# Optimization experiments

Hardware: AMD Instinct MI355X
Metric: run time of the kernel (lower is better)

## Reference

```python
import jax, jax.numpy as jnp
import numpy as np

B, N, K, A = 2, 4096, 20, 12
DIMS = [32, 64, 128, 256, 512]
POOL_RATE, POOL_K = 4, 4


def knn_index(v, k):
    # v: (b, n, 3) -> (b, n, k) nearest neighbors, self excluded
    d2 = jnp.sum(v * v, axis=-1)
    dist = d2[:, :, None] + d2[:, None, :] - 2.0 * jnp.einsum('bnd,bmd->bnm', v, v)
    _, idx = jax.lax.top_k(-dist, k + 1)
    return idx[:, :, 1:]


def gather_pos(v, idx):
    return jax.vmap(lambda vv, ii: vv[ii])(v, idx)  # (b, n, k, 3)


def gather_fea(fm, idx):
    return jax.vmap(lambda f, ii: f[:, ii, :])(fm, idx)  # (b, c, n, k, a)


def nbr_dirs(v, idx):
    d = gather_pos(v, idx) - v[:, :, None, :]
    return d / (jnp.linalg.norm(d, axis=-1, keepdims=True) + 1e-8)


def conv_surface(idx, v, K0):
    # K0: (C0, A, 3) learned direction kernels; output (b, C0, n, A)
    d = nbr_dirs(v, idx)  # (b,n,k,3)
    theta = jax.nn.relu(jnp.einsum('bnkd,cad->bnkca', d, K0))
    return jnp.transpose(jnp.max(theta, axis=2), (0, 2, 1, 3))


def equi_conv(idx, v, fm, dirs, Wc, bc, Ws):
    # fm: (b, cin, n, a) -> (b, cout, n, a)
    d = nbr_dirs(v, idx)
    theta = jax.nn.relu(jnp.einsum('bnkd,ad->bnka', d, dirs))  # (b,n,k,a)
    fn = gather_fea(fm, idx)  # (b,cin,n,k,a)
    fs = jnp.einsum('bcnka,co->bonka', fn, Ws) * theta[:, None]
    fs = jnp.max(fs, axis=3)  # max over neighbors -> (b,cout,n,a)
    fc = jnp.einsum('bcna,co->bona', fm, Wc) + bc[None, :, None, None]
    return fc + fs


def batchnorm(x, g, b):
    m = jnp.mean(x, axis=(0, 2, 3), keepdims=True)
    var = jnp.var(x, axis=(0, 2, 3), keepdims=True)
    return (x - m) * jax.lax.rsqrt(var + 1e-5) * g[None, :, None, None] + b[None, :, None, None]


def pool(v, fm):
    idx = knn_index(v, POOL_K)
    fn = jnp.max(gather_fea(fm, idx), axis=3)
    fm_p = jnp.maximum(fm, fn)
    sel = jnp.arange(0, v.shape[1], POOL_RATE)  # strided subsample
    return v[:, sel], fm_p[:, :, sel]


def fea_of(fm):
    return jnp.transpose(jnp.max(fm, axis=-1), (0, 2, 1))  # (b,n,c)


def setup_inputs() -> dict:
    key = jax.random.key(0)
    ks = iter(jax.random.split(key, 32))
    p = {'vertices': jax.random.normal(next(ks), (B, N, 3), jnp.float32)}
    p['K0'] = jax.random.normal(next(ks), (DIMS[0], A, 3), jnp.float32) * 0.1
    for i, (ci, co) in enumerate(zip(DIMS[:4], DIMS[1:]), start=1):
        s = 1.0 / np.sqrt(ci).astype(np.float32)
        p[f'dirs{i}'] = jax.random.normal(next(ks), (A, 3), jnp.float32) * 0.1
        p[f'Wc{i}'] = jax.random.normal(next(ks), (ci, co), jnp.float32) * s
        p[f'bc{i}'] = jnp.zeros((co,), jnp.float32)
        p[f'Ws{i}'] = jax.random.normal(next(ks), (ci, co), jnp.float32) * s
    for i, c in enumerate([DIMS[1], DIMS[2], DIMS[3]], start=1):
        p[f'g{i}'] = jnp.ones((c,), jnp.float32)
        p[f'b{i}'] = jnp.zeros((c,), jnp.float32)
    return p


def reference(vertices, K0, dirs1, Wc1, bc1, Ws1, dirs2, Wc2, bc2, Ws2,
              dirs3, Wc3, bc3, Ws3, dirs4, Wc4, bc4, Ws4,
              g1, b1, g2, b2, g3, b3):
    idx = knn_index(vertices, K)
    fm0 = jax.nn.relu(conv_surface(idx, vertices, K0))
    fm1 = jax.nn.relu(batchnorm(equi_conv(idx, vertices, fm0, dirs1, Wc1, bc1, Ws1), g1, b1))
    v1, fmp1 = pool(vertices, fm1)
    idx1 = knn_index(v1, min(K, v1.shape[1] // 8))
    fm2 = jax.nn.relu(batchnorm(equi_conv(idx1, v1, fmp1, dirs2, Wc2, bc2, Ws2), g2, b2))
    fm3 = jax.nn.relu(batchnorm(equi_conv(idx1, v1, fm2, dirs3, Wc3, bc3, Ws3), g3, b3))
    v2, fmp2 = pool(v1, fm3)
    idx2 = knn_index(v2, min(K, v2.shape[1] // 8))
    fm4 = equi_conv(idx2, v2, fmp2, dirs4, Wc4, bc4, Ws4)
    return fea_of(fm0), fea_of(fm1), fea_of(fm2), fea_of(fm3), fea_of(fm4)
```

## Files before the change

### kernel.cpp

```cpp
#include <hip/hip_runtime.h>
#include <hip/hip_bf16.h>
#include <math.h>

typedef unsigned short u16;
typedef unsigned long long u64;
#define DEV static __device__ __forceinline__

constexpr int Bz = 2, N0 = 4096, N1 = 1024, N2 = 256, KNN = 20, NA = 12;
constexpr int C0 = 32, C1 = 64, C2 = 128, C3 = 256, C4 = 512;
constexpr int BNG = 32;

constexpr size_t OFF_V0F   = 0;
constexpr size_t OFF_V1F   = 32768;
constexpr size_t OFF_V2F   = 40960;
constexpr size_t OFF_K0F   = 43008;
constexpr size_t OFF_DIRS  = 44160;
constexpr size_t OFF_WC    = 44304;
constexpr size_t OFF_WS    = 218384;
constexpr size_t OFF_BC    = 392464;
constexpr size_t OFF_BN    = 393424;
constexpr size_t OFF_FLAG  = 394832;
constexpr size_t OFF_IDX0  = 394848;
constexpr size_t OFF_IDX1  = 558688;
constexpr size_t OFF_IDX2  = 599648;
constexpr size_t OFF_PART  = 609888;
constexpr size_t PART_SZ   = 28672;
constexpr size_t OFF_HALF  = OFF_PART + PART_SZ;

constexpr size_t HA = 0;
constexpr size_t HB = 3145728;
constexpr size_t HG = 9437184;
constexpr size_t HP = HG + 3145728;

constexpr size_t OUT0 = 0;
constexpr size_t OUT1 = OUT0 + (size_t)Bz*N0*C0;
constexpr size_t OUT2 = OUT1 + (size_t)Bz*N0*C1;
constexpr size_t OUT3 = OUT2 + (size_t)Bz*N1*C2;
constexpr size_t OUT4 = OUT3 + (size_t)Bz*N1*C3;

DEV float b2f(u16 v) { return __uint_as_float(((unsigned int)v) << 16); }
DEV u16 f2b(float f) {
  unsigned int u = __float_as_uint(f);
  unsigned int lsb = (u >> 16) & 1u;
  return (u16)((u + 0x7fffu + lsb) >> 16);
}
DEV unsigned packb(float a, float b) {
  return (unsigned)f2b(a) | ((unsigned)f2b(b) << 16);
}

DEV u64 shflx64(u64 v, int m) {
  int lo = __shfl_xor((int)(unsigned)v, m, 64);
  int hi = __shfl_xor((int)(unsigned)(v >> 32), m, 64);
  return ((u64)(unsigned)hi << 32) | (unsigned)lo;
}
DEV int mbcnt64(u64 m) {
  return __builtin_amdgcn_mbcnt_hi((unsigned)(m >> 32),
         __builtin_amdgcn_mbcnt_lo((unsigned)m, 0));
}

DEV void st12(float* dst, const float* v) {
  float4 a{v[0],v[1],v[2],v[3]}, b{v[4],v[5],v[6],v[7]}, c{v[8],v[9],v[10],v[11]};
  ((float4*)dst)[0] = a; ((float4*)dst)[1] = b; ((float4*)dst)[2] = c;
}
DEV void st12(u16* dst, const float* v) {
  uint2 a{packb(v[0],v[1]), packb(v[2],v[3])};
  uint2 b{packb(v[4],v[5]), packb(v[6],v[7])};
  uint2 c{packb(v[8],v[9]), packb(v[10],v[11])};
  ((uint2*)dst)[0] = a; ((uint2*)dst)[1] = b; ((uint2*)dst)[2] = c;
}

struct InPtrs { const void* p[24]; };

__global__ void eq_convert_all(InPtrs in, float* ws) {
  __shared__ int sflag;
  {
    const u16* v = (const u16*)in.p[0];
    if (threadIdx.x < 64) {
      int bad = 0;
      #pragma unroll
      for (int j = 0; j < 4; ++j) {
        unsigned u = v[threadIdx.x*4 + j];
        int ex = (u >> 7) & 0xFF;
        bad += (((u & 0x7FFFu) != 0u) && (ex < 64 || ex > 191)) ? 1 : 0;
      }
      int tot = bad;
      #pragma unroll
      for (int s = 32; s > 0; s >>= 1) tot += __shfl_xor(tot, s, 64);
      if (threadIdx.x == 0) sflag = (tot >= 8) ? 1 : 0;
    }
    __syncthreads();
  }
  int f32mode = sflag;
  int t = blockIdx.x * blockDim.x + threadIdx.x;
  if (t < Bz*N0) {
    float x, y, z;
    if (f32mode) { const float* v = (const float*)in.p[0]; x=v[t*3]; y=v[t*3+1]; z=v[t*3+2]; }
    else { const u16* v = (const u16*)in.p[0]; x=b2f(v[t*3]); y=b2f(v[t*3+1]); z=b2f(v[t*3+2]); }
    float4 o; o.x=x; o.y=y; o.z=z; o.w=(x*x + y*y) + z*z;
    ((float4*)(ws + OFF_V0F))[t] = o;
    int b = t / N0, i = t % N0;
    if ((i & 3) == 0)  ((float4*)(ws + OFF_V1F))[b*N1 + (i >> 2)] = o;
    if ((i & 15) == 0) ((float4*)(ws + OFF_V2F))[b*N2 + (i >> 4)] = o;
    return;
  }
  int r = t - Bz*N0;
  if (r >= 351312) {
    int z = r - 351312;
    if (z < (int)PART_SZ) ws[OFF_PART + z] = 0.f;
    return;
  }
  const int cnt[23] = {1152, 36,2048,64,2048, 36,8192,128,8192,
                       36,32768,256,32768, 36,131072,512,131072,
                       64,64,128,128,256,256};
  const size_t off[23] = {OFF_K0F,
    OFF_DIRS+0,   OFF_WC+0,     OFF_BC+0,   OFF_WS+0,
    OFF_DIRS+36,  OFF_WC+2048,  OFF_BC+64,  OFF_WS+2048,
    OFF_DIRS+72,  OFF_WC+10240, OFF_BC+192, OFF_WS+10240,
    OFF_DIRS+108, OFF_WC+43008, OFF_BC+448, OFF_WS+43008,
    OFF_BN+0, OFF_BN+64, OFF_BN+128, OFF_BN+256, OFF_BN+384, OFF_BN+640};
  for (int i = 0; i < 23; ++i) {
    if (r < cnt[i]) {
      float val = f32mode ? ((const float*)in.p[i+1])[r] : b2f(((const u16*)in.p[i+1])[r]);
      ws[off[i] + r] = val;
      return;
    }
    r -= cnt[i];
  }
}

DEV unsigned cand_ud(const float4 vq, const float4 vc) {
  float dt = fmaf(vq.x, vc.x, fmaf(vq.y, vc.y, vq.z*vc.z));
  float d  = fmaf(-2.0f, dt, vq.w + vc.w);
  unsigned u = __float_as_uint(d);
  return u ^ ((unsigned)(((int)u) >> 31) | 0x80000000u);
}

#define INSA(u,c) do { bool lt1=(u)<dA1, lt2=(u)<dA2, lt3=(u)<dA3, lt4=(u)<dA4; \
  dA4=lt3?dA3:(lt4?(u):dA4); iA4=lt3?iA3:(lt4?(c):iA4); \
  dA3=lt2?dA2:(lt3?(u):dA3); iA3=lt2?iA2:(lt3?(c):iA3); \
  dA2=lt1?dA1:(lt2?(u):dA2); iA2=lt1?iA1:(lt2?(c):iA2); \
  dA1=lt1?(u):dA1;           iA1=lt1?(c):iA1; } while(0)
#define INSB(u,c) do { bool lt1=(u)<dB1, lt2=(u)<dB2, lt3=(u)<dB3, lt4=(u)<dB4; \
  dB4=lt3?dB3:(lt4?(u):dB4); iB4=lt3?iB3:(lt4?(c):iB4); \
  dB3=lt2?dB2:(lt3?(u):dB3); iB3=lt2?iB2:(lt3?(c):iB3); \
  dB2=lt1?dB1:(lt2?(u):dB2); iB2=lt1?iB1:(lt2?(c):iB2); \
  dB1=lt1?(u):dB1;           iB1=lt1?(c):iB1; } while(0)

#define CMP1(uu,cc) do { bool sel=(uu)<=p; u64 m=__ballot(sel); \
  int pos = base2 + mbcnt64(m); \
  if (sel && pos < 128) selw[pos] = ((u64)(uu) << 32) | (unsigned)(cc); \
  base2 += __popcll(m); } while(0)

template<int NPTS>
DEV void knn_body(int blk, const float4* __restrict__ vf, int* __restrict__ idx_out,
                  char* smem) {
  constexpr int CPL = NPTS/64;
  constexpr int HC  = CPL/2;
  int wave = threadIdx.x >> 6, lane = threadIdx.x & 63;
  u64* selw = (u64*)smem + wave*128;
  int* extrw = (int*)(smem + 4*128*8) + wave*24;
  int qid = blk*4 + wave;
  int b = qid / NPTS, q = qid % NPTS;
  const float4* vb = vf + (size_t)b*NPTS;
  float4 vq = vb[q];

  unsigned dA1=~0u,dA2=~0u,dA3=~0u,dA4=~0u; int iA1=0,iA2=0,iA3=0,iA4=0;
  unsigned dB1=~0u,dB2=~0u,dB3=~0u,dB4=~0u; int iB1=0,iB2=0,iB3=0,iB4=0;

  if (CPL >= 8) {
    for (int jb = 0; jb < CPL; jb += 8) {
      int base = jb*64 + lane;
      float4 c0 = vb[base];
      float4 c1 = vb[base + 64];
      float4 c2 = vb[base + 128];
      float4 c3 = vb[base + 192];
      float4 c4 = vb[base + 256];
      float4 c5 = vb[base + 320];
      float4 c6 = vb[base + 384];
      float4 c7 = vb[base + 448];
      unsigned u0 = cand_ud(vq, c0);
      unsigned u1 = cand_ud(vq, c1);
      unsigned u2 = cand_ud(vq, c2);
      unsigned u3 = cand_ud(vq, c3);
      unsigned u4 = cand_ud(vq, c4);
      unsigned u5 = cand_ud(vq, c5);
      unsigned u6 = cand_ud(vq, c6);
      unsigned u7 = cand_ud(vq, c7);
      INSA(u0, base);       INSB(u1, base + 64);
      INSA(u2, base + 128); INSB(u3, base + 192);
      INSA(u4, base + 256); INSB(u5, base + 320);
      INSA(u6, base + 384); INSB(u7, base + 448);
    }
  } else {
    int base = lane;
    float4 c0 = vb[base];
    float4 c1 = vb[base + 64];
    float4 c2 = vb[base + 128];
    float4 c3 = vb[base + 192];
    unsigned u0 = cand_ud(vq, c0);
    unsigned u1 = cand_ud(vq, c1);
    unsigned u2 = cand_ud(vq, c2);
    unsigned u3 = cand_ud(vq, c3);
    INSA(u0, base);       INSB(u1, base + 64);
    INSA(u2, base + 128); INSB(u3, base + 192);
  }

  unsigned p = 0;
  for (int bit = 31; bit >= 0; --bit) {
    unsigned T = p | (1u << bit);
    int cnt = __popcll(__ballot(dA1 < T)) + __popcll(__ballot(dA2 < T))
            + __popcll(__ballot(dA3 < T)) + __popcll(__ballot(dA4 < T))
            + __popcll(__ballot(dB1 < T)) + __popcll(__ballot(dB2 < T))
            + __popcll(__ballot(dB3 < T)) + __popcll(__ballot(dB4 < T));
    if (cnt < KNN+1) p = T;
  }
  size_t obase = (size_t)qid*KNN;
  bool need_fb = (HC > 4) &&
                 ((__ballot(dA4 <= p) | __ballot(dB4 <= p)) != 0ULL);

  if (!need_fb) {
    bool pA1=dA1<=p, pA2=dA2<=p, pA3=dA3<=p, pA4=dA4<=p;
    bool pB1=dB1<=p, pB2=dB2<=p, pB3=dB3<=p, pB4=dB4<=p;
    u64 m1=__ballot(pA1), m2=__ballot(pA2), m3=__ballot(pA3), m4=__ballot(pA4);
    u64 m5=__ballot(pB1), m6=__ballot(pB2), m7=__ballot(pB3), m8=__ballot(pB4);
    int c1=__popcll(m1), c2=__popcll(m2), c3=__popcll(m3), c4=__popcll(m4);
    int c5=__popcll(m5), c6=__popcll(m6), c7=__popcll(m7), c8=__popcll(m8);
    int S = ((c1+c2)+(c3+c4)) + ((c5+c6)+(c7+c8));
    if (S > 127) need_fb = true;
    else {
      int o1=c1, o2=o1+c2, o3=o2+c3, o4=o3+c4, o5=o4+c5, o6=o5+c6, o7=o6+c7;
      if (pA1) selw[mbcnt64(m1)]      = ((u64)dA1 << 32) | (unsigned)iA1;
      if (pA2) selw[o1 + mbcnt64(m2)] = ((u64)dA2 << 32) | (unsigned)iA2;
      if (pA3) selw[o2 + mbcnt64(m3)] = ((u64)dA3 << 32) | (unsigned)iA3;
      if (pA4) selw[o3 + mbcnt64(m4)] = ((u64)dA4 << 32) | (unsigned)iA4;
      if (pB1) selw[o4 + mbcnt64(m5)] = ((u64)dB1 << 32) | (unsigned)iB1;
      if (pB2) selw[o5 + mbcnt64(m6)] = ((u64)dB2 << 32) | (unsigned)iB2;
      if (pB3) selw[o6 + mbcnt64(m7)] = ((u64)dB3 << 32) | (unsigned)iB3;
      if (pB4) selw[o7 + mbcnt64(m8)] = ((u64)dB4 << 32) | (unsigned)iB4;
      for (int sl = lane; sl < S; sl += 64) {
        u64 mykey = selw[sl];
        int rank = 0;
        for (int j2 = 0; j2 < S; ++j2) rank += (selw[j2] < mykey) ? 1 : 0;
        if (rank >= 1 && rank <= KNN)
          idx_out[obase + rank - 1] = (int)(unsigned)(mykey & 0xFFFFFFFFu);
      }
    }
  }
  if (need_fb && CPL >= 8) {
    int base2 = 0;
    for (int jb = 0; jb < CPL; jb += 8) {
      int bidx = jb*64 + lane;
      float4 c0 = vb[bidx];
      float4 c1 = vb[bidx + 64];
      float4 c2 = vb[bidx + 128];
      float4 c3 = vb[bidx + 192];
      float4 c4 = vb[bidx + 256];
      float4 c5 = vb[bidx + 320];
      float4 c6 = vb[bidx + 384];
      float4 c7 = vb[bidx + 448];
      unsigned u0 = cand_ud(vq, c0);
      unsigned u1 = cand_ud(vq, c1);
      unsigned u2 = cand_ud(vq, c2);
      unsigned u3 = cand_ud(vq, c3);
      unsigned u4 = cand_ud(vq, c4);
      unsigned u5 = cand_ud(vq, c5);
      unsigned u6 = cand_ud(vq, c6);
      unsigned u7 = cand_ud(vq, c7);
      CMP1(u0, bidx);       CMP1(u1, bidx + 64);
      CMP1(u2, bidx + 128); CMP1(u3, bidx + 192);
      CMP1(u4, bidx + 256); CMP1(u5, bidx + 320);
      CMP1(u6, bidx + 384); CMP1(u7, bidx + 448);
    }
    if (base2 <= 127) {
      int S = base2;
      for (int sl = lane; sl < S; sl += 64) {
        u64 mykey = selw[sl];
        int rank = 0;
        for (int j2 = 0; j2 < S; ++j2) rank += (selw[j2] < mykey) ? 1 : 0;
        if (rank >= 1 && rank <= KNN)
          idx_out[obase + rank - 1] = (int)(unsigned)(mykey & 0xFFFFFFFFu);
      }
    } else {
      const u64 KINF = ~0ULL;
      u64 K1=KINF, K2=KINF, K3=KINF, K4=KINF;
      for (int j = 0; j < CPL; ++j) {
        int c = j*64 + lane;
        u64 k = ((u64)cand_ud(vq, vb[c]) << 32) | (unsigned)c;
        bool lt1 = k < K1, lt2 = k < K2, lt3 = k < K3, lt4 = k < K4;
        K4 = lt3 ? K3 : (lt4 ? k : K4);
        K3 = lt2 ? K2 : (lt3 ? k : K3);
        K2 = lt1 ? K1 : (lt2 ? k : K2);
        K1 = lt1 ? k  : K1;
      }
      for (int r = 0; r < KNN+1; ++r) {
        u64 g = K1;
        #pragma unroll
        for (int s = 32; s; s >>= 1) { u64 o = shflx64(g, s); g = (o < g) ? o : g; }
        int gidx = (int)(unsigned)(g & 0xFFFFFFFFu);
        if (lane == 0) {
          extrw[r] = gidx;
          if (r > 0) idx_out[obase + r - 1] = gidx;
        }
        if (r < KNN && lane == (gidx & 63)) {
          K1 = K2; K2 = K3; K3 = K4; K4 = KINF;
          if (K1 == KINF) {
            for (int j = 0; j < CPL; ++j) {
              int c = j*64 + lane;
              u64 k = ((u64)cand_ud(vq, vb[c]) << 32) | (unsigned)c;
              bool ex = false;
              for (int e = 0; e <= r; ++e) ex |= (extrw[e] == c);
              if (!ex) {
                bool lt1 = k < K1, lt2 = k < K2, lt3 = k < K3, lt4 = k < K4;
                K4 = lt3 ? K3 : (lt4 ? k : K4);
                K3 = lt2 ? K2 : (lt3 ? k : K3);
                K2 = lt1 ? K1 : (lt2 ? k : K2);
                K1 = lt1 ? k  : K1;
              }
            }
          }
        }
      }
    }
  }
}

__global__ __launch_bounds__(256) void eq_knn_all(
    const float4* __restrict__ v0, int* __restrict__ i0,
    const float4* __restrict__ v1, int* __restrict__ i1,
    const float4* __restrict__ v2, int* __restrict__ i2) {
  __shared__ __align__(16) char smem[4*128*8 + 4*24*4];
  int blk = blockIdx.x;
  constexpr int NB0 = Bz*N0/4, NB1 = Bz*N1/4;
  if (blk < NB0)            knn_body<N0>(blk, v0, i0, smem);
  else if (blk < NB0+NB1)   knn_body<N1>(blk - NB0, v1, i1, smem);
  else                      knn_body<N2>(blk - NB0 - NB1, v2, i2, smem);
}

__global__ __launch_bounds__(128) void eq_conv_surface(
    const float4* __restrict__ v0f, const int* __restrict__ idx0,
    const float* __restrict__ K0f, u16* __restrict__ fm0, float* __restrict__ out0) {
  int bq = blockIdx.x;
  int b = bq >> 12;
  __shared__ float dk[KNN][3];
  __shared__ float row[C0*NA];
  int tid = threadIdx.x;
  if (tid < KNN) {
    int m = idx0[(size_t)bq*KNN + tid];
    float4 vq = v0f[bq];
    float4 vm = v0f[(size_t)b*N0 + m];
    float dx = vm.x - vq.x, dy = vm.y - vq.y, dz = vm.z - vq.z;
    float nrm = sqrtf((dx*dx + dy*dy) + dz*dz) + 1e-8f;
    dk[tid][0] = dx/nrm; dk[tid][1] = dy/nrm; dk[tid][2] = dz/nrm;
  }
  __syncthreads();
  for (int t4 = tid; t4 < C0*NA/4; t4 += 128) {
    const float* kd = K0f + (size_t)t4*12;
    float4 k0 = *(const float4*)(kd);
    float4 k1 = *(const float4*)(kd + 4);
    float4 k2 = *(const float4*)(kd + 8);
    float m0=0.f, m1=0.f, m2=0.f, m3=0.f;
    #pragma unroll
    for (int k = 0; k < KNN; ++k) {
      float dx = dk[k][0], dy = dk[k][1], dz = dk[k][2];
      m0 = fmaxf(m0, (dx*k0.x + dy*k0.y) + dz*k0.z);
      m1 = fmaxf(m1, (dx*k0.w + dy*k1.x) + dz*k1.y);
      m2 = fmaxf(m2, (dx*k1.z + dy*k1.w) + dz*k2.x);
      m3 = fmaxf(m3, (dx*k2.y + dy*k2.z) + dz*k2.w);
    }
    uint2 r; r.x = packb(m0, m1); r.y = packb(m2, m3);
    ((uint2*)fm0)[(size_t)bq*(C0*NA/4) + t4] = r;
    row[4*t4+0] = m0; row[4*t4+1] = m1; row[4*t4+2] = m2; row[4*t4+3] = m3;
  }
  __syncthreads();
  if (tid < C0) {
    float m = row[tid*NA];
    #pragma unroll
    for (int a = 1; a < NA; ++a) m = fmaxf(m, row[tid*NA + a]);
    out0[(size_t)bq*C0 + tid] = m;
  }
}

template<int CI, int CO, typename TO>
__global__ __launch_bounds__(256) void eq_linear4(
    const u16* __restrict__ in, const float* __restrict__ Wc,
    const float* __restrict__ Ws, const float* __restrict__ bias,
    TO* __restrict__ fc, u16* __restrict__ g) {
  constexpr int PPB = 512 / CO;
  constexpr int RS = CI*NA + 4;
  __shared__ float lds[PPB*RS];
  int tid = threadIdx.x;
  int mat = blockIdx.x & 1;
  int pt0 = (blockIdx.x >> 1) * PPB;
  constexpr int E = PPB*CI*NA;
  for (int t = tid; t < E; t += 256) {
    int pt = t / (CI*NA), r = t % (CI*NA);
    lds[pt*RS + r] = b2f(in[((size_t)(pt0+pt))*CI*NA + r]);
  }
  __syncthreads();
  constexpr int TPP = CO/2;
  int opair = tid % TPP, pt = tid / TPP;
  int o0 = opair*2;
  const float* W = mat ? Ws : Wc;
  const float* row = lds + pt*RS;
  float a0[NA], a1[NA];
  #pragma unroll
  for (int a = 0; a < NA; ++a) { a0[a]=0.f; a1[a]=0.f; }
  #pragma unroll 4
  for (int c = 0; c < CI; ++c) {
    float2 w2 = *(const float2*)(W + (size_t)c*CO + o0);
    float4 i0 = *(const float4*)(row + c*NA);
    float4 i1 = *(const float4*)(row + c*NA + 4);
    float4 i2 = *(const float4*)(row + c*NA + 8);
    float iv[NA] = {i0.x,i0.y,i0.z,i0.w, i1.x,i1.y,i1.z,i1.w, i2.x,i2.y,i2.z,i2.w};
    #pragma unroll
    for (int a = 0; a < NA; ++a) {
      a0[a] += iv[a]*w2.x; a1[a] += iv[a]*w2.y;
    }
  }
  size_t ptg = pt0 + pt;
  if (mat == 0) {
    float b0 = bias[o0], b1 = bias[o0+1];
    #pragma unroll
    for (int a = 0; a < NA; ++a) { a0[a] += b0; a1[a] += b1; }
    st12(fc + ((size_t)ptg*CO + o0)*NA, a0);
    st12(fc + ((size_t)ptg*CO + o0 + 1)*NA, a1);
  } else {
    st12(g + ((size_t)ptg*CO + o0)*NA, a0);
    st12(g + ((size_t)ptg*CO + o0 + 1)*NA, a1);
  }
}

__global__ __launch_bounds__(256) void eq_fsmax(
    const u16* __restrict__ g, const float4* __restrict__ vf,
    const float* __restrict__ dirs, const int* __restrict__ idx,
    u16* __restrict__ out, float* __restrict__ part, int npts, int co) {
  int bq = blockIdx.x;
  int b = bq / npts;
  __shared__ float th[KNN*NA];
  __shared__ float dk[KNN][3];
  __shared__ int nb[KNN];
  __shared__ float sstat[2][C3];
  int tid = threadIdx.x;
  if (tid < KNN) {
    int m = idx[(size_t)bq*KNN + tid];
    nb[tid] = m;
    float4 vq = vf[bq];
    float4 vm = vf[(size_t)b*npts + m];
    float dx = vm.x - vq.x, dy = vm.y - vq.y, dz = vm.z - vq.z;
    float nrm = sqrtf((dx*dx + dy*dy) + dz*dz) + 1e-8f;
    dk[tid][0] = dx/nrm; dk[tid][1] = dy/nrm; dk[tid][2] = dz/nrm;
  }
  sstat[0][tid] = 0.f; sstat[1][tid] = 0.f;
  __syncthreads();
  if (tid < KNN*NA) {
    int k = tid / NA, a = tid % NA;
    float s = (dk[k][0]*dirs[a*3] + dk[k][1]*dirs[a*3+1]) + dk[k][2]*dirs[a*3+2];
    th[tid] = fmaxf(s, 0.f);
  }
  __syncthreads();
  int quarter = co*NA/4;
  uint2* dst = (uint2*)(out + (size_t)bq*co*NA);
  const uint2* gb = (const uint2*)(g + (size_t)b*npts*co*NA);
  for (int t4 = tid; t4 < quarter; t4 += 256) {
    int a = (4*t4) % NA;
    const float* tha = th + a;
    float m0=-3.0e38f, m1=-3.0e38f, m2=-3.0e38f, m3=-3.0e38f;
    #pragma unroll 5
    for (int k = 0; k < KNN; ++k) {
      uint2 pv = gb[(size_t)nb[k]*quarter + t4];
      float4 tv = *(const float4*)(tha + k*NA);
      m0 = fmaxf(m0, tv.x*b2f((u16)(pv.x)));
      m1 = fmaxf(m1, tv.y*b2f((u16)(pv.x >> 16)));
      m2 = fmaxf(m2, tv.z*b2f((u16)(pv.y)));
      m3 = fmaxf(m3, tv.w*b2f((u16)(pv.y >> 16)));
    }
    uint2 d = dst[t4];
    float v0 = b2f((u16)d.x) + m0;
    float v1 = b2f((u16)(d.x >> 16)) + m1;
    float v2 = b2f((u16)d.y) + m2;
    float v3 = b2f((u16)(d.y >> 16)) + m3;
    uint2 r; r.x = packb(v0, v1); r.y = packb(v2, v3);
    dst[t4] = r;
    int ch = t4 / 3;
    atomicAdd(&sstat[0][ch], (v0 + v1) + (v2 + v3));
    atomicAdd(&sstat[1][ch], (v0*v0 + v1*v1) + (v2*v2 + v3*v3));
  }
  __syncthreads();
  if (tid < co) {
    float* pg = part + (size_t)(bq & (BNG-1))*2*co;
    atomicAdd(&pg[tid], sstat[0][tid]);
    atomicAdd(&pg[co + tid], sstat[1][tid]);
  }
}

template<int SPL>
__global__ __launch_bounds__(256) void eq_fsmax_fea(
    const u16* __restrict__ g, const float* __restrict__ fcin,
    const float4* __restrict__ vf, const float* __restrict__ dirs,
    const int* __restrict__ idx, float* __restrict__ outfea,
    int npts, int co) {
  constexpr int CHUNK = C4 / SPL;
  int part = blockIdx.x % SPL;
  int bq = blockIdx.x / SPL;
  int b = bq / npts;
  __shared__ float th[KNN*NA];
  __shared__ float dk[KNN][3];
  __shared__ int nb[KNN];
  __shared__ float row[CHUNK*NA];
  int tid = threadIdx.x;
  if (tid < KNN) {
    int m = idx[(size_t)bq*KNN + tid];
    nb[tid] = m;
    float4 vq = vf[bq];
    float4 vm = vf[(size_t)b*npts + m];
    float dx = vm.x - vq.x, dy = vm.y - vq.y, dz = vm.z - vq.z;
    float nrm = sqrtf((dx*dx + dy*dy) + dz*dz) + 1e-8f;
    dk[tid][0] = dx/nrm; dk[tid][1] = dy/nrm; dk[tid][2] = dz/nrm;
  }
  __syncthreads();
  if (tid < KNN*NA) {
    int k = tid / NA, a = tid % NA;
    float s = (dk[k][0]*dirs[a*3] + dk[k][1]*dirs[a*3+1]) + dk[k][2]*dirs[a*3+2];
    th[tid] = fmaxf(s, 0.f);
  }
  __syncthreads();
  int o0 = part * CHUNK;
  const float4* fcr = (const float4*)(fcin + ((size_t)bq*co + o0)*NA);
  const uint2* gb = (const uint2*)(g + (size_t)b*npts*co*NA + (size_t)o0*NA);
  int gquarter = co*NA/4;
  for (int t4 = tid; t4 < CHUNK*NA/4; t4 += 256) {
    int a = (4*t4) % NA;
    const float* tha = th + a;
    float m0=-3.0e38f, m1=-3.0e38f, m2=-3.0e38f, m3=-3.0e38f;
    #pragma unroll 5
    for (int k = 0; k < KNN; ++k) {
      uint2 pv = gb[(size_t)nb[k]*gquarter + t4];
      float4 tv = *(const float4*)(tha + k*NA);
      m0 = fmaxf(m0, tv.x*b2f((u16)(pv.x)));
      m1 = fmaxf(m1, tv.y*b2f((u16)(pv.x >> 16)));
      m2 = fmaxf(m2, tv.z*b2f((u16)(pv.y)));
      m3 = fmaxf(m3, tv.w*b2f((u16)(pv.y >> 16)));
    }
    float4 fc4 = fcr[t4];
    row[4*t4+0] = fc4.x + m0;
    row[4*t4+1] = fc4.y + m1;
    row[4*t4+2] = fc4.z + m2;
    row[4*t4+3] = fc4.w + m3;
  }
  __syncthreads();
  for (int o = tid; o < CHUNK; o += 256) {
    float m = row[o*NA];
    #pragma unroll
    for (int a = 1; a < NA; ++a) m = fmaxf(m, row[o*NA + a]);
    outfea[(size_t)bq*co + o0 + o] = m;
  }
}

__global__ __launch_bounds__(256) void eq_bnrelu_fea(
    u16* __restrict__ fm, const float* __restrict__ part,
    const float* __restrict__ gamma, const float* __restrict__ beta,
    float* __restrict__ outfea, int npts, int co) {
  int bq = blockIdx.x;
  int tid = threadIdx.x;
  __shared__ float sc[C3], sh[C3];
  __shared__ float row[C3*NA];
  for (int o = tid; o < co; o += 256) {
    float s = 0.f, s2 = 0.f;
    for (int g = 0; g < BNG; ++g) {
      s  += part[(size_t)g*2*co + o];
      s2 += part[(size_t)g*2*co + co + o];
    }
    float cnt = (float)(Bz*npts*NA);
    float mean = s / cnt;
    float var = fmaxf(s2 / cnt - mean*mean, 0.f);
    float inv = 1.0f / sqrtf(var + 1e-5f);
    sc[o] = gamma[o] * inv;
    sh[o] = beta[o] - mean * gamma[o] * inv;
  }
  __syncthreads();
  uint2* p = (uint2*)(fm + (size_t)bq*co*NA);
  int quarter = co*NA/4;
  for (int t4 = tid; t4 < quarter; t4 += 256) {
    int o = (4*t4) / NA;
    float s = sc[o], h = sh[o];
    uint2 pv = p[t4];
    float v0 = fmaxf(b2f((u16)pv.x)*s + h, 0.f);
    float v1 = fmaxf(b2f((u16)(pv.x >> 16))*s + h, 0.f);
    float v2 = fmaxf(b2f((u16)pv.y)*s + h, 0.f);
    float v3 = fmaxf(b2f((u16)(pv.y >> 16))*s + h, 0.f);
    uint2 r; r.x = packb(v0, v1); r.y = packb(v2, v3);
    p[t4] = r;
    row[4*t4+0] = v0; row[4*t4+1] = v1; row[4*t4+2] = v2; row[4*t4+3] = v3;
  }
  __syncthreads();
  for (int o = tid; o < co; o += 256) {
    float m = row[o*NA];
    #pragma unroll
    for (int a = 1; a < NA; ++a) m = fmaxf(m, row[o*NA + a]);
    outfea[(size_t)bq*co + o] = m;
  }
}

__global__ __launch_bounds__(256) void eq_bnfea_pool(
    const u16* __restrict__ fm, const float* __restrict__ part,
    const float* __restrict__ gamma, const float* __restrict__ beta,
    const int* __restrict__ idx, float* __restrict__ outfea,
    u16* __restrict__ fmp, int npts, int co) {
  int bq = blockIdx.x;
  int b = bq / npts, q = bq % npts;
  int tid = threadIdx.x;
  __shared__ float sc[C3], sh[C3];
  __shared__ float row[C3*NA];
  __shared__ int nb[4];
  for (int o = tid; o < co; o += 256) {
    float s = 0.f, s2 = 0.f;
    for (int g = 0; g < BNG; ++g) {
      s  += part[(size_t)g*2*co + o];
      s2 += part[(size_t)g*2*co + co + o];
    }
    float cnt = (float)(Bz*npts*NA);
    float mean = s / cnt;
    float var = fmaxf(s2 / cnt - mean*mean, 0.f);
    float inv = 1.0f / sqrtf(var + 1e-5f);
    sc[o] = gamma[o] * inv;
    sh[o] = beta[o] - mean * gamma[o] * inv;
  }
  bool do_pool = ((q & 3) == 0);
  if (do_pool && tid < 4) nb[tid] = idx[(size_t)bq*KNN + tid];
  __syncthreads();
  int quarter = co*NA/4;
  const uint2* own = (const uint2*)(fm + (size_t)bq*co*NA);
  const uint2* base = (const uint2*)(fm + (size_t)b*npts*co*NA);
  uint2* dst = (uint2*)(fmp + ((size_t)b*(npts/4) + (q >> 2))*co*NA);
  for (int t4 = tid; t4 < quarter; t4 += 256) {
    int o = (4*t4) / NA;
    float s = sc[o], h = sh[o];
    uint2 pv = own[t4];
    float v0 = fmaxf(b2f((u16)pv.x)*s + h, 0.f);
    float v1 = fmaxf(b2f((u16)(pv.x >> 16))*s + h, 0.f);
    float v2 = fmaxf(b2f((u16)pv.y)*s + h, 0.f);
    float v3 = fmaxf(b2f((u16)(pv.y >> 16))*s + h, 0.f);
    row[4*t4+0] = v0; row[4*t4+1] = v1; row[4*t4+2] = v2; row[4*t4+3] = v3;
    if (do_pool) {
      float m0=v0, m1=v1, m2=v2, m3=v3;
      #pragma unroll
      for (int kk = 0; kk < 4; ++kk) {
        uint2 w = base[(size_t)nb[kk]*quarter + t4];
        m0 = fmaxf(m0, fmaxf(b2f((u16)w.x)*s + h, 0.f));
        m1 = fmaxf(m1, fmaxf(b2f((u16)(w.x >> 16))*s + h, 0.f));
        m2 = fmaxf(m2, fmaxf(b2f((u16)w.y)*s + h, 0.f));
        m3 = fmaxf(m3, fmaxf(b2f((u16)(w.y >> 16))*s + h, 0.f));
      }
      uint2 r; r.x = packb(m0, m1); r.y = packb(m2, m3);
      dst[t4] = r;
    }
  }
  __syncthreads();
  for (int o = tid; o < co; o += 256) {
    float m = row[o*NA];
    #pragma unroll
    for (int a = 1; a < NA; ++a) m = fmaxf(m, row[o*NA + a]);
    outfea[(size_t)bq*co + o] = m;
  }
}

extern "C" void kernel_launch(void* const* d_in, const int* in_sizes, int n_in,
                              void* d_out, int out_size, void* d_ws, size_t ws_size,
                              hipStream_t stream) {
  float* ws = (float*)d_ws;
  float* out = (float*)d_out;
  u16* arena = (u16*)(ws + OFF_HALF);

  InPtrs ip;
  for (int i = 0; i < 24; ++i) ip.p[i] = d_in[i];

  float4* v0f = (float4*)(ws + OFF_V0F);
  float4* v1f = (float4*)(ws + OFF_V1F);
  float4* v2f = (float4*)(ws + OFF_V2F);
  int* idx0 = (int*)(ws + OFF_IDX0);
  int* idx1 = (int*)(ws + OFF_IDX1);
  int* idx2 = (int*)(ws + OFF_IDX2);
  u16* bufA = arena + HA;
  u16* bufB = arena + HB;
  float* fc4f = (float*)(arena + HB);
  u16* bufG = arena + HG;
  u16* bufP = arena + HP;
  float* partA = ws + OFF_PART;
  float* partB = ws + OFF_PART + 4096;
  float* partC = ws + OFF_PART + 12288;
  const float* DIRS = ws + OFF_DIRS;

  {
    int total = Bz*N0 + 351312 + (int)PART_SZ;
    eq_convert_all<<<(total + 255)/256, 256, 0, stream>>>(ip, ws);
  }

  eq_knn_all<<<Bz*N0/4 + Bz*N1/4 + Bz*N2/4, 256, 0, stream>>>(v0f, idx0, v1f, idx1, v2f, idx2);
  eq_conv_surface<<<Bz*N0, 128, 0, stream>>>(v0f, idx0, ws + OFF_K0F, bufA, out + OUT0);

  eq_linear4<C0, C1, u16><<<(Bz*N0/8)*2, 256, 0, stream>>>(bufA, ws + OFF_WC + 0, ws + OFF_WS + 0,
                                                           ws + OFF_BC + 0, bufB, bufG);
  eq_fsmax<<<Bz*N0, 256, 0, stream>>>(bufG, v0f, DIRS + 0, idx0, bufB, partA, N0, C1);
  eq_bnfea_pool<<<Bz*N0, 256, 0, stream>>>(bufB, partA, ws + OFF_BN + 0, ws + OFF_BN + 64,
                                           idx0, out + OUT1, bufP, N0, C1);

  eq_linear4<C1, C2, u16><<<(Bz*N1/4)*2, 256, 0, stream>>>(bufP, ws + OFF_WC + 2048, ws + OFF_WS + 2048,
                                                           ws + OFF_BC + 64, bufA, bufG);
  eq_fsmax<<<Bz*N1, 256, 0, stream>>>(bufG, v1f, DIRS + 36, idx1, bufA, partB, N1, C2);
  eq_bnrelu_fea<<<Bz*N1, 256, 0, stream>>>(bufA, partB, ws + OFF_BN + 128, ws + OFF_BN + 256,
                                           out + OUT2, N1, C2);

  eq_linear4<C2, C3, u16><<<(Bz*N1/2)*2, 256, 0, stream>>>(bufA, ws + OFF_WC + 10240, ws + OFF_WS + 10240,
                                                           ws + OFF_BC + 192, bufB, bufG);
  eq_fsmax<<<Bz*N1, 256, 0, stream>>>(bufG, v1f, DIRS + 72, idx1, bufB, partC, N1, C3);
  eq_bnfea_pool<<<Bz*N1, 256, 0, stream>>>(bufB, partC, ws + OFF_BN + 384, ws + OFF_BN + 640,
                                           idx1, out + OUT3, bufP, N1, C3);

  eq_linear4<C3, C4, float><<<(Bz*N2)*2, 256, 0, stream>>>(bufP, ws + OFF_WC + 43008, ws + OFF_WS + 43008,
                                                           ws + OFF_BC + 448, fc4f, bufG);
  eq_fsmax_fea<4><<<Bz*N2*4, 256, 0, stream>>>(bufG, fc4f, v2f, DIRS + 108, idx2, out + OUT4, N2, C4);
}
```

Before: 442.9 us.

## Use bf16 MFMA with hi/lo weight split for equivariant linear layers

Replaces the scalar FP32 per-point linear kernels with MFMA 16x16x32 bf16 matrix-core kernels. A new prep kernel transposes each weight matrix and splits it into bf16 high and low parts, so two MFMAs per k-step keep near-fp32 accuracy on the weight side. Input tiles are staged in LDS, transposed to an (angle, point) by channel layout. Points per block change for most layers, and the extra weight-prep launch plus the scattered scalar output stores add cost.

```diff
diff --git a/kernel.cpp b/kernel.cpp
--- a/kernel.cpp
+++ b/kernel.cpp
@@ -31,6 +31,7 @@
 constexpr size_t HB = 3145728;
 constexpr size_t HG = 9437184;
 constexpr size_t HP = HG + 3145728;
+constexpr size_t WTO = 15728640;
 
 constexpr size_t OUT0 = 0;
 constexpr size_t OUT1 = OUT0 + (size_t)Bz*N0*C0;
@@ -126,6 +127,28 @@
     }
     r -= cnt[i];
   }
+}
+
+__global__ void eq_wprep(const float* __restrict__ ws,
+    u16* __restrict__ ch, u16* __restrict__ cl,
+    u16* __restrict__ sh, u16* __restrict__ sl) {
+  int e = blockIdx.x*256 + threadIdx.x;
+  if (e >= 174080) return;
+  const int co[4] = {64,128,256,512};
+  const int ci[4] = {32,64,128,256};
+  const int off[4] = {0,2048,10240,43008};
+  int li = 0, loc = e;
+  if (e >= 43008) { li = 3; loc = e - 43008; }
+  else if (e >= 10240) { li = 2; loc = e - 10240; }
+  else if (e >= 2048) { li = 1; loc = e - 2048; }
+  int c = loc / co[li], o = loc % co[li];
+  size_t dst = (size_t)off[li] + (size_t)o*ci[li] + c;
+  float wc = ws[OFF_WC + e];
+  u16 h = f2b(wc); u16 l = f2b(wc - b2f(h));
+  ch[dst] = h; cl[dst] = l;
+  float wv = ws[OFF_WS + e];
+  h = f2b(wv); l = f2b(wv - b2f(h));
+  sh[dst] = h; sl[dst] = l;
 }
 
 DEV unsigned cand_ud(const float4 vq, const float4 vc) {
@@ -380,53 +403,66 @@
   }
 }
 
-template<int CI, int CO, typename TO>
-__global__ __launch_bounds__(256) void eq_linear4(
-    const u16* __restrict__ in, const float* __restrict__ Wc,
-    const float* __restrict__ Ws, const float* __restrict__ bias,
-    TO* __restrict__ fc, u16* __restrict__ g) {
-  constexpr int PPB = 512 / CO;
-  constexpr int RS = CI*NA + 4;
-  __shared__ float lds[PPB*RS];
+typedef __attribute__((ext_vector_type(8))) short bf16x8;
+typedef __attribute__((ext_vector_type(4))) float f32x4;
+
+DEV void store1(float* p, float v) { *p = v; }
+DEV void store1(u16* p, float v) { *p = f2b(v); }
+
+template<int CI, int CO, int PT, typename TO>
+__global__ __launch_bounds__(256) void eq_linear_mfma(
+    const u16* __restrict__ in,
+    const u16* __restrict__ wc_hi, const u16* __restrict__ wc_lo,
+    const u16* __restrict__ ws_hi, const u16* __restrict__ ws_lo,
+    const float* __restrict__ bias, TO* __restrict__ fc, u16* __restrict__ g) {
+  constexpr int MR = 12*PT;
+  constexpr int TM = MR/16;
+  constexpr int TN = CO/16;
+  constexpr int KF = CI/32;
+  constexpr int RS = CI + 8;
+  __shared__ u16 As[MR*RS];
   int tid = threadIdx.x;
   int mat = blockIdx.x & 1;
-  int pt0 = (blockIdx.x >> 1) * PPB;
-  constexpr int E = PPB*CI*NA;
-  for (int t = tid; t < E; t += 256) {
-    int pt = t / (CI*NA), r = t % (CI*NA);
-    lds[pt*RS + r] = b2f(in[((size_t)(pt0+pt))*CI*NA + r]);
-  }
-  __syncthreads();
-  constexpr int TPP = CO/2;
-  int opair = tid % TPP, pt = tid / TPP;
-  int o0 = opair*2;
-  const float* W = mat ? Ws : Wc;
-  const float* row = lds + pt*RS;
-  float a0[NA], a1[NA];
-  #pragma unroll
-  for (int a = 0; a < NA; ++a) { a0[a]=0.f; a1[a]=0.f; }
-  #pragma unroll 4
-  for (int c = 0; c < CI; ++c) {
-    float2 w2 = *(const float2*)(W + (size_t)c*CO + o0);
-    float4 i0 = *(const float4*)(row + c*NA);
-    float4 i1 = *(const float4*)(row + c*NA + 4);
-    float4 i2 = *(const float4*)(row + c*NA + 8);
-    float iv[NA] = {i0.x,i0.y,i0.z,i0.w, i1.x,i1.y,i1.z,i1.w, i2.x,i2.y,i2.z,i2.w};
+  int pt0 = (blockIdx.x >> 1) * PT;
+  constexpr int EU = PT*CI*12/2;
+  const unsigned* inw = (const unsigned*)(in + (size_t)pt0*CI*12);
+  for (int t = tid; t < EU; t += 256) {
+    unsigned v = inw[t];
+    int e = 2*t;
+    int pt = e / (CI*12), r = e % (CI*12);
+    int c = r / 12, a = r % 12;
+    As[(a*PT + pt)*RS + c] = (u16)v;
+    As[((a+1)*PT + pt)*RS + c] = (u16)(v >> 16);
+  }
+  __syncthreads();
+  int wave = tid >> 6, lane = tid & 63;
+  int lr = lane & 15;
+  int lk = lane >> 4;
+  const u16* Whi = mat ? ws_hi : wc_hi;
+  const u16* Wlo = mat ? ws_lo : wc_lo;
+  for (int tp = wave; tp < TM*TN; tp += 4) {
+    int mt = tp % TM, nt = tp / TM;
+    int n0 = nt*16;
+    f32x4 acc = {0.f, 0.f, 0.f, 0.f};
     #pragma unroll
-    for (int a = 0; a < NA; ++a) {
-      a0[a] += iv[a]*w2.x; a1[a] += iv[a]*w2.y;
-    }
-  }
-  size_t ptg = pt0 + pt;
-  if (mat == 0) {
-    float b0 = bias[o0], b1 = bias[o0+1];
+    for (int kf = 0; kf < KF; ++kf) {
+      bf16x8 af = *(const bf16x8*)&As[(mt*16 + lr)*RS + kf*32 + lk*8];
+      bf16x8 bh = *(const bf16x8*)&Whi[(size_t)(n0 + lr)*CI + kf*32 + lk*8];
+      bf16x8 bl = *(const bf16x8*)&Wlo[(size_t)(n0 + lr)*CI + kf*32 + lk*8];
+      acc = __builtin_amdgcn_mfma_f32_16x16x32_bf16(af, bh, acc, 0, 0, 0);
+      acc = __builtin_amdgcn_mfma_f32_16x16x32_bf16(af, bl, acc, 0, 0, 0);
+    }
+    int n = n0 + lr;
+    float bv = (mat == 0) ? bias[n] : 0.f;
     #pragma unroll
-    for (int a = 0; a < NA; ++a) { a0[a] += b0; a1[a] += b1; }
-    st12(fc + ((size_t)ptg*CO + o0)*NA, a0);
-    st12(fc + ((size_t)ptg*CO + o0 + 1)*NA, a1);
-  } else {
-    st12(g + ((size_t)ptg*CO + o0)*NA, a0);
-    st12(g + ((size_t)ptg*CO + o0 + 1)*NA, a1);
+    for (int j = 0; j < 4; ++j) {
+      int m = mt*16 + lk*4 + j;
+      int a = m / PT, pt = m % PT;
+      float v = acc[j] + bv;
+      size_t oaddr = ((size_t)(pt0 + pt)*CO + n)*NA + a;
+      if (mat == 0) store1(fc + oaddr, v);
+      else          store1(g + oaddr, v);
+    }
   }
 }
 
@@ -685,6 +721,10 @@
   float* fc4f = (float*)(arena + HB);
   u16* bufG = arena + HG;
   u16* bufP = arena + HP;
+  u16* wch = arena + WTO;
+  u16* wcl = wch + 174080;
+  u16* wsh = wcl + 174080;
+  u16* wsl = wsh + 174080;
   float* partA = ws + OFF_PART;
   float* partB = ws + OFF_PART + 4096;
   float* partC = ws + OFF_PART + 12288;
@@ -694,29 +734,30 @@
     int total = Bz*N0 + 351312 + (int)PART_SZ;
     eq_convert_all<<<(total + 255)/256, 256, 0, stream>>>(ip, ws);
   }
+  eq_wprep<<<(174080 + 255)/256, 256, 0, stream>>>(ws, wch, wcl, wsh, wsl);
 
   eq_knn_all<<<Bz*N0/4 + Bz*N1/4 + Bz*N2/4, 256, 0, stream>>>(v0f, idx0, v1f, idx1, v2f, idx2);
   eq_conv_surface<<<Bz*N0, 128, 0, stream>>>(v0f, idx0, ws + OFF_K0F, bufA, out + OUT0);
 
-  eq_linear4<C0, C1, u16><<<(Bz*N0/8)*2, 256, 0, stream>>>(bufA, ws + OFF_WC + 0, ws + OFF_WS + 0,
-                                                           ws + OFF_BC + 0, bufB, bufG);
+  eq_linear_mfma<C0, C1, 8, u16><<<(Bz*N0/8)*2, 256, 0, stream>>>(
+      bufA, wch + 0, wcl + 0, wsh + 0, wsl + 0, ws + OFF_BC + 0, bufB, bufG);
   eq_fsmax<<<Bz*N0, 256, 0, stream>>>(bufG, v0f, DIRS + 0, idx0, bufB, partA, N0, C1);
   eq_bnfea_pool<<<Bz*N0, 256, 0, stream>>>(bufB, partA, ws + OFF_BN + 0, ws + OFF_BN + 64,
                                            idx0, out + OUT1, bufP, N0, C1);
 
-  eq_linear4<C1, C2, u16><<<(Bz*N1/4)*2, 256, 0, stream>>>(bufP, ws + OFF_WC + 2048, ws + OFF_WS + 2048,
-                                                           ws + OFF_BC + 64, bufA, bufG);
+  eq_linear_mfma<C1, C2, 8, u16><<<(Bz*N1/8)*2, 256, 0, stream>>>(
+      bufP, wch + 2048, wcl + 2048, wsh + 2048, wsl + 2048, ws + OFF_BC + 64, bufA, bufG);
   eq_fsmax<<<Bz*N1, 256, 0, stream>>>(bufG, v1f, DIRS + 36, idx1, bufA, partB, N1, C2);
   eq_bnrelu_fea<<<Bz*N1, 256, 0, stream>>>(bufA, partB, ws + OFF_BN + 128, ws + OFF_BN + 256,
                                            out + OUT2, N1, C2);
 
-  eq_linear4<C2, C3, u16><<<(Bz*N1/2)*2, 256, 0, stream>>>(bufA, ws + OFF_WC + 10240, ws + OFF_WS + 10240,
-                                                           ws + OFF_BC + 192, bufB, bufG);
+  eq_linear_mfma<C2, C3, 8, u16><<<(Bz*N1/8)*2, 256, 0, stream>>>(
+      bufA, wch + 10240, wcl + 10240, wsh + 10240, wsl + 10240, ws + OFF_BC + 192, bufB, bufG);
   eq_fsmax<<<Bz*N1, 256, 0, stream>>>(bufG, v1f, DIRS + 72, idx1, bufB, partC, N1, C3);
   eq_bnfea_pool<<<Bz*N1, 256, 0, stream>>>(bufB, partC, ws + OFF_BN + 384, ws + OFF_BN + 640,
                                            idx1, out + OUT3, bufP, N1, C3);
 
-  eq_linear4<C3, C4, float><<<(Bz*N2)*2, 256, 0, stream>>>(bufP, ws + OFF_WC + 43008, ws + OFF_WS + 43008,
-                                                           ws + OFF_BC + 448, fc4f, bufG);
+  eq_linear_mfma<C3, C4, 4, float><<<(Bz*N2/4)*2, 256, 0, stream>>>(
+      bufP, wch + 43008, wcl + 43008, wsh + 43008, wsl + 43008, ws + OFF_BC + 448, fc4f, bufG);
   eq_fsmax_fea<4><<<Bz*N2*4, 256, 0, stream>>>(bufG, fc4f, v2f, DIRS + 108, idx2, out + OUT4, N2, C4);
 }
```

Measured after the change: 474.4 us. 1.07x slower.
